# Kernel optimization log

Hardware: AMD Instinct MI355X
Metric: run time of the kernel (lower is better)

## Reference

```python
import jax, jax.numpy as jnp
import numpy as np

EPS = 1e-6


def _layernorm(x, g, b):
    mu = jnp.mean(x, axis=-1, keepdims=True)
    var = jnp.mean((x - mu) ** 2, axis=-1, keepdims=True)
    return (x - mu) * jax.lax.rsqrt(var + EPS) * g + b


def _sinusoidal_pe(seq_len, d_model):
    pos = jnp.arange(seq_len, dtype=jnp.float32)[:, None]
    div = jnp.exp(jnp.arange(0, d_model, 2, dtype=jnp.float32) * (-np.log(10000.0) / d_model))
    pe = jnp.zeros((seq_len, d_model), dtype=jnp.float32)
    pe = pe.at[:, 0::2].set(jnp.sin(pos * div))
    pe = pe.at[:, 1::2].set(jnp.cos(pos * div))
    return pe


def setup_inputs() -> dict:
    key = jax.random.key(0)
    ks = jax.random.split(key, 6)
    B, S, D, H = 4, 4096, 1024, 16
    std = 0.02
    return {
        "x": jax.random.normal(ks[0], (B, S, D), jnp.float32),
        "ln1_g": jnp.ones((D,), jnp.float32),
        "ln1_b": jnp.zeros((D,), jnp.float32),
        "w_qkv": jax.random.normal(ks[1], (D, 3 * D), jnp.float32) * std,
        "w_out": jax.random.normal(ks[2], (D, D), jnp.float32) * std,
        "b_out": jnp.zeros((D,), jnp.float32),
        "ln2_g": jnp.ones((D,), jnp.float32),
        "ln2_b": jnp.zeros((D,), jnp.float32),
        "w1": jax.random.normal(ks[3], (D, 2 * D), jnp.float32) * std,
        "b1": jnp.zeros((2 * D,), jnp.float32),
        "w2": jax.random.normal(ks[4], (2 * D, 2 * D), jnp.float32) * std,
        "b2": jnp.zeros((2 * D,), jnp.float32),
        "w3": jax.random.normal(ks[5], (2 * D, D), jnp.float32) * std,
        "b3": jnp.zeros((D,), jnp.float32),
    }


def reference(x, ln1_g, ln1_b, w_qkv, w_out, b_out, ln2_g, ln2_b, w1, b1, w2, b2, w3, b3):
    B, S, D = x.shape
    H = 16
    dh = D // H  # dim_head = 64

    h = _layernorm(x, ln1_g, ln1_b)
    h = h + _sinusoidal_pe(S, D)[None]  # space_dim == 1 -> sinusoidal PE

    # linear (kernelized, non-causal) self-attention: efficient-attention style
    qkv = h @ w_qkv  # [B,S,3D]
    q, k, v = jnp.split(qkv, 3, axis=-1)
    to_heads = lambda t: t.reshape(B, S, H, dh).transpose(0, 2, 1, 3)  # [B,H,S,dh]
    q, k, v = to_heads(q), to_heads(k), to_heads(v)
    q = jax.nn.softmax(q, axis=-1) * (dh ** -0.5)
    k = jax.nn.softmax(k, axis=2)  # softmax over sequence
    context = jnp.einsum('bhnd,bhne->bhde', k, v)  # [B,H,dh,dh]
    attn = jnp.einsum('bhnd,bhde->bhne', q, context)  # [B,H,S,dh]
    attn = attn.transpose(0, 2, 1, 3).reshape(B, S, D)
    attn = attn @ w_out + b_out

    x = x + attn  # residual (dropout p=0)

    y = _layernorm(x, ln2_g, ln2_b)
    y = jax.nn.gelu(y @ w1 + b1, approximate=False)
    y = jax.nn.gelu(y @ w2 + b2, approximate=False)
    y = y @ w3 + b3
    return x + y
```

## Files before the change

### kernel.cpp

```cpp
#include <hip/hip_runtime.h>
#include <cstdint>
#include <cstddef>

#define BB 4
#define SS 4096
#define DD 1024
#define HH 16
#define MM (BB*SS)

typedef __bf16 bf16x8 __attribute__((ext_vector_type(8)));
typedef float  f32x4  __attribute__((ext_vector_type(4)));

__device__ __forceinline__ float b2f(unsigned short h){
    union { unsigned int u; float f; } c; c.u = ((unsigned int)h) << 16; return c.f;
}
__device__ __forceinline__ float b2f_u(unsigned int u16){
    union { unsigned int u; float f; } c; c.u = u16 << 16; return c.f;
}
__device__ __forceinline__ unsigned short f2b(float f){
    union { float f; unsigned int u; } c; c.f = f;
    unsigned int u = c.u + 0x7FFFu + ((c.u >> 16) & 1u);
    return (unsigned short)(u >> 16);
}

__global__ __launch_bounds__(256) void transpose_cvt_all(
        const float* __restrict__ wqkv, const float* __restrict__ wout,
        const float* __restrict__ w1,   const float* __restrict__ w2,
        const float* __restrict__ w3,
        unsigned short* __restrict__ dqkv, unsigned short* __restrict__ dout,
        unsigned short* __restrict__ d1,   unsigned short* __restrict__ d2,
        unsigned short* __restrict__ d3)
{
    int id = blockIdx.x;
    const float* src; unsigned short* dst; int K, N, bx, by;
    if (id < 3072)       { src=wqkv; dst=dqkv; K=1024; N=3072; int r=id;        bx=r%96; by=r/96; }
    else if (id < 4096)  { src=wout; dst=dout; K=1024; N=1024; int r=id-3072;   bx=r%32; by=r/32; }
    else if (id < 6144)  { src=w1;   dst=d1;   K=1024; N=2048; int r=id-4096;   bx=r%64; by=r/64; }
    else if (id < 10240) { src=w2;   dst=d2;   K=2048; N=2048; int r=id-6144;   bx=r%64; by=r/64; }
    else                 { src=w3;   dst=d3;   K=2048; N=1024; int r=id-10240;  bx=r%32; by=r/32; }

    __shared__ float tile[32][33];
    int kb = by*32, nb = bx*32;
    int tx = threadIdx.x & 31, ty = threadIdx.x >> 5;
    for(int i=0;i<32;i+=8) tile[ty+i][tx] = src[(size_t)(kb+ty+i)*N + nb+tx];
    __syncthreads();
    for(int i=0;i<32;i+=8) dst[(size_t)(nb+ty+i)*K + kb+tx] = f2b(tile[tx][ty+i]);
}

template<int INBF>
__global__ __launch_bounds__(256) void ln_kernel(const void* __restrict__ xin,
                                                 const float* __restrict__ g,
                                                 const float* __restrict__ bta,
                                                 unsigned short* __restrict__ out,
                                                 int add_pe){
    int row = blockIdx.x;
    int t = threadIdx.x;
    float4 v;
    if (INBF == 0) {
        v = ((const float4*)((const float*)xin + (size_t)row*DD))[t];
    } else {
        ushort4 u = ((const ushort4*)((const unsigned short*)xin + (size_t)row*DD))[t];
        v.x = b2f(u.x); v.y = b2f(u.y); v.z = b2f(u.z); v.w = b2f(u.w);
    }
    float s = v.x+v.y+v.z+v.w;
    float q = v.x*v.x+v.y*v.y+v.z*v.z+v.w*v.w;
    for(int off=32; off>0; off>>=1){ s += __shfl_xor(s, off); q += __shfl_xor(q, off); }
    __shared__ float red[8];
    int wv = t>>6, ln = t&63;
    if(ln==0){ red[wv] = s; red[4+wv] = q; }
    __syncthreads();
    s = red[0]+red[1]+red[2]+red[3];
    q = red[4]+red[5]+red[6]+red[7];
    float mu = s * (1.0f/1024.0f);
    float var = q * (1.0f/1024.0f) - mu*mu;
    float rs = rsqrtf(var + 1e-6f);
    int d0 = t*4;
    float4 gg = ((const float4*)g)[t];
    float4 bb = ((const float4*)bta)[t];
    float o0 = (v.x-mu)*rs*gg.x + bb.x;
    float o1 = (v.y-mu)*rs*gg.y + bb.y;
    float o2 = (v.z-mu)*rs*gg.z + bb.z;
    float o3 = (v.w-mu)*rs*gg.w + bb.w;
    if(add_pe){
        int sidx = row & (SS-1);
        const float cfac = -0.008994473019508968f;
        float a0 = (float)sidx * expf(cfac * (float)(d0));
        float a1 = (float)sidx * expf(cfac * (float)(d0 + 2));
        o0 += sinf(a0); o1 += cosf(a0);
        o2 += sinf(a1); o3 += cosf(a1);
    }
    ushort4 o;
    o.x = f2b(o0); o.y = f2b(o1); o.z = f2b(o2); o.w = f2b(o3);
    *(ushort4*)(out + (size_t)row*DD + d0) = o;
}

template<int EPI>
__global__ __launch_bounds__(256, 4) void gemm_bt(
        const unsigned short* __restrict__ A,
        const unsigned short* __restrict__ Bt,
        void* __restrict__ Cout,
        const float* __restrict__ bias,
        const void* __restrict__ resid,
        int M, int N, int K)
{
    __shared__ __align__(16) unsigned short lA[128*64];
    __shared__ __align__(16) unsigned short lB[128*64];
    const int tid  = threadIdx.x;
    const int lane = tid & 63;
    const int wave = tid >> 6;
    const int quad = lane >> 4;
    const int l16  = lane & 15;
    const int wr = wave >> 1, wc = wave & 1;

    int gn  = gridDim.x;
    int lin = blockIdx.y * gn + blockIdx.x;
    int xcd = lin & 7;
    int j   = lin >> 3;
    int mt  = xcd + 8*(j/gn);
    int nt  = j - (j/gn)*gn;
    const int m0 = mt * 128;
    const int n0 = nt * 128;

    f32x4 acc[4][4] = {};

    for (int k0 = 0; k0 < K; k0 += 64) {
        __syncthreads();
        #pragma unroll
        for (int i = 0; i < 4; i++) {
            int c   = tid + 256*i;
            int row = c >> 3;
            int kc  = ((c & 7) ^ (row & 7)) << 3;
            const unsigned short* gA = A  + (size_t)(m0 + row) * K + k0 + kc;
            const unsigned short* gB = Bt + (size_t)(n0 + row) * K + k0 + kc;
            char* lpA = ((char*)lA) + (wave<<10) + (i<<12);
            char* lpB = ((char*)lB) + (wave<<10) + (i<<12);
            __builtin_amdgcn_global_load_lds((const __attribute__((address_space(1))) void*)gA,
                                             (__attribute__((address_space(3))) void*)lpA, 16, 0, 0);
            __builtin_amdgcn_global_load_lds((const __attribute__((address_space(1))) void*)gB,
                                             (__attribute__((address_space(3))) void*)lpB, 16, 0, 0);
        }
        __syncthreads();
        #pragma unroll
        for (int kk = 0; kk < 2; kk++) {
            bf16x8 af[4], bfr[4];
            #pragma unroll
            for (int mi = 0; mi < 4; mi++) {
                int row = wr*64 + mi*16 + l16;
                int kb  = (kk*64 + quad*16) ^ ((row & 7) << 4);
                af[mi] = *(const bf16x8*)((const char*)lA + row*128 + kb);
            }
            #pragma unroll
            for (int ni = 0; ni < 4; ni++) {
                int row = wc*64 + ni*16 + l16;
                int kb  = (kk*64 + quad*16) ^ ((row & 7) << 4);
                bfr[ni] = *(const bf16x8*)((const char*)lB + row*128 + kb);
            }
            #pragma unroll
            for (int mi = 0; mi < 4; mi++)
                #pragma unroll
                for (int ni = 0; ni < 4; ni++)
                    acc[mi][ni] = __builtin_amdgcn_mfma_f32_16x16x32_bf16(af[mi], bfr[ni], acc[mi][ni], 0, 0, 0);
        }
    }

    #pragma unroll
    for (int mi = 0; mi < 4; mi++) {
        #pragma unroll
        for (int r = 0; r < 4; r++) {
            int grow = m0 + wr*64 + mi*16 + quad*4 + r;
            #pragma unroll
            for (int ni = 0; ni < 4; ni++) {
                int gcol = n0 + wc*64 + ni*16 + l16;
                float v = acc[mi][ni][r];
                size_t idx = (size_t)grow * N + gcol;
                if (EPI == 0) {
                    ((unsigned short*)Cout)[idx] = f2b(v);
                } else if (EPI == 1) {
                    v += bias[gcol];
                    v = 0.5f * v * (1.0f + erff(v * 0.70710678118654752f));
                    ((unsigned short*)Cout)[idx] = f2b(v);
                } else if (EPI == 2) {
                    v += bias[gcol] + ((const float*)resid)[idx];
                    ((unsigned short*)Cout)[idx] = f2b(v);
                } else {
                    v += bias[gcol] + b2f(((const unsigned short*)resid)[idx]);
                    ((float*)Cout)[idx] = v;
                }
            }
        }
    }
}

__global__ __launch_bounds__(256) void ctx_partial(const unsigned short* __restrict__ qkv,
                                                   float* __restrict__ EP,
                                                   float* __restrict__ CS){
    int sc = blockIdx.x, h = blockIdx.y, b = blockIdx.z;
    int t = threadIdx.x;
    __shared__ __align__(16) float kl[64][64];
    __shared__ __align__(16) float vl[64][64];
    __shared__ float csred[4][64];
    float acc[4][4] = {};
    float cspart = 0.0f;
    int e4 = (t & 15) * 4, d4 = (t >> 4) * 4;
    int dcol = t & 63, schunk = t >> 6;
    for(int s0 = 0; s0 < 256; s0 += 64){
        __syncthreads();
        #pragma unroll
        for(int j=0;j<2;j++){
            int lin = t + 256*j;
            int row = lin >> 3;
            int c8  = (lin & 7) * 8;
            size_t gr = (size_t)(b*SS + sc*256 + s0 + row);
            uint4 kv = *(const uint4*)(qkv + gr*3072 + DD + h*64 + c8);
            float4 ka, kb2;
            ka.x = expf(b2f_u(kv.x & 0xFFFFu)); ka.y = expf(b2f_u(kv.x >> 16));
            ka.z = expf(b2f_u(kv.y & 0xFFFFu)); ka.w = expf(b2f_u(kv.y >> 16));
            kb2.x = expf(b2f_u(kv.z & 0xFFFFu)); kb2.y = expf(b2f_u(kv.z >> 16));
            kb2.z = expf(b2f_u(kv.w & 0xFFFFu)); kb2.w = expf(b2f_u(kv.w >> 16));
            *(float4*)&kl[row][c8]   = ka;
            *(float4*)&kl[row][c8+4] = kb2;
            uint4 vv = *(const uint4*)(qkv + gr*3072 + 2*DD + h*64 + c8);
            float4 va, vb;
            va.x = b2f_u(vv.x & 0xFFFFu); va.y = b2f_u(vv.x >> 16);
            va.z = b2f_u(vv.y & 0xFFFFu); va.w = b2f_u(vv.y >> 16);
            vb.x = b2f_u(vv.z & 0xFFFFu); vb.y = b2f_u(vv.z >> 16);
            vb.z = b2f_u(vv.w & 0xFFFFu); vb.w = b2f_u(vv.w >> 16);
            *(float4*)&vl[row][c8]   = va;
            *(float4*)&vl[row][c8+4] = vb;
        }
        __syncthreads();
        #pragma unroll
        for(int i=0;i<16;i++) cspart += kl[schunk*16+i][dcol];
        for(int s=0;s<64;s++){
            float4 k4 = *(const float4*)&kl[s][d4];
            float4 v4 = *(const float4*)&vl[s][e4];
            acc[0][0] += k4.x*v4.x; acc[0][1] += k4.x*v4.y; acc[0][2] += k4.x*v4.z; acc[0][3] += k4.x*v4.w;
            acc[1][0] += k4.y*v4.x; acc[1][1] += k4.y*v4.y; acc[1][2] += k4.y*v4.z; acc[1][3] += k4.y*v4.w;
            acc[2][0] += k4.z*v4.x; acc[2][1] += k4.z*v4.y; acc[2][2] += k4.z*v4.z; acc[2][3] += k4.z*v4.w;
            acc[3][0] += k4.w*v4.x; acc[3][1] += k4.w*v4.y; acc[3][2] += k4.w*v4.z; acc[3][3] += k4.w*v4.w;
        }
    }
    int slot = (b*HH + h)*16 + sc;
    float* ep = EP + (size_t)slot*4096;
    #pragma unroll
    for(int i=0;i<4;i++)
        *(float4*)&ep[(d4+i)*64 + e4] = *(float4*)&acc[i][0];
    csred[schunk][dcol] = cspart;
    __syncthreads();
    if(t < 64) CS[slot*64 + t] = csred[0][t]+csred[1][t]+csred[2][t]+csred[3][t];
}

__global__ __launch_bounds__(256) void ctx_reduce(const float* __restrict__ EP,
                                                  const float* __restrict__ CS,
                                                  float* __restrict__ CTXF){
    int bh = blockIdx.x;
    int t = threadIdx.x;
    int d = t >> 2, e0 = (t & 3) * 16;
    float cs = 0.0f;
    #pragma unroll
    for(int sl=0; sl<16; sl++) cs += CS[(bh*16+sl)*64 + d];
    float inv = 1.0f/cs;
    #pragma unroll
    for(int i=0;i<16;i++){
        float s = 0.0f;
        #pragma unroll
        for(int sl=0; sl<16; sl++) s += EP[(size_t)(bh*16+sl)*4096 + d*64 + e0 + i];
        CTXF[(size_t)bh*4096 + d*64 + e0 + i] = s * inv;
    }
}

__global__ __launch_bounds__(256) void attn_heads(const unsigned short* __restrict__ qkv,
                                                  const float* __restrict__ CTXF,
                                                  unsigned short* __restrict__ abuf){
    int rg = blockIdx.x, h = blockIdx.y;
    int b = rg >> 6;
    int t = threadIdx.x;
    __shared__ __align__(16) float cl[64][64];
    __shared__ __align__(16) float qlT[64*68];
    const float* cb = CTXF + (size_t)(b*HH + h)*4096;
    for(int j=0;j<4;j++){
        int lin = t + 256*j;
        ((float4*)cl)[lin] = ((const float4*)cb)[lin];
    }
    {
        int r = t >> 2, seg = (t & 3) * 16;
        const unsigned short* qp = qkv + (size_t)(rg*64 + r)*3072 + h*64 + seg;
        float vals[16];
        float m = -1e30f;
        #pragma unroll
        for(int u=0; u<4; u++){
            ushort4 qv = *(const ushort4*)(qp + u*4);
            vals[u*4+0]=b2f(qv.x); vals[u*4+1]=b2f(qv.y); vals[u*4+2]=b2f(qv.z); vals[u*4+3]=b2f(qv.w);
        }
        #pragma unroll
        for(int i=0;i<16;i++) m = fmaxf(m, vals[i]);
        m = fmaxf(m, __shfl_xor(m, 1));
        m = fmaxf(m, __shfl_xor(m, 2));
        float ssum = 0.0f;
        #pragma unroll
        for(int i=0;i<16;i++){ vals[i] = expf(vals[i]-m); ssum += vals[i]; }
        ssum += __shfl_xor(ssum, 1);
        ssum += __shfl_xor(ssum, 2);
        float scl = 0.125f/ssum;
        #pragma unroll
        for(int i=0;i<16;i++) qlT[(seg+i)*68 + r] = vals[i]*scl;
    }
    __syncthreads();
    int e4 = (t & 15) * 4, r4 = (t >> 4) * 4;
    float acc[4][4] = {};
    for(int d=0; d<64; d++){
        float4 q4 = *(const float4*)&qlT[d*68 + r4];
        float4 c4 = *(const float4*)&cl[d][e4];
        acc[0][0] += q4.x*c4.x; acc[0][1] += q4.x*c4.y; acc[0][2] += q4.x*c4.z; acc[0][3] += q4.x*c4.w;
        acc[1][0] += q4.y*c4.x; acc[1][1] += q4.y*c4.y; acc[1][2] += q4.y*c4.z; acc[1][3] += q4.y*c4.w;
        acc[2][0] += q4.z*c4.x; acc[2][1] += q4.z*c4.y; acc[2][2] += q4.z*c4.z; acc[2][3] += q4.z*c4.w;
        acc[3][0] += q4.w*c4.x; acc[3][1] += q4.w*c4.y; acc[3][2] += q4.w*c4.z; acc[3][3] += q4.w*c4.w;
    }
    #pragma unroll
    for(int i=0;i<4;i++){
        ushort4 o;
        o.x = f2b(acc[i][0]); o.y = f2b(acc[i][1]); o.z = f2b(acc[i][2]); o.w = f2b(acc[i][3]);
        *(ushort4*)(abuf + (size_t)(rg*64 + r4 + i)*DD + h*64 + e4) = o;
    }
}

extern "C" void kernel_launch(void* const* d_in, const int* in_sizes, int n_in,
                              void* d_out, int out_size, void* d_ws, size_t ws_size,
                              hipStream_t stream)
{
    const float* x     = (const float*)d_in[0];
    const float* ln1_g = (const float*)d_in[1];
    const float* ln1_b = (const float*)d_in[2];
    const float* w_qkv = (const float*)d_in[3];
    const float* w_out = (const float*)d_in[4];
    const float* b_out = (const float*)d_in[5];
    const float* ln2_g = (const float*)d_in[6];
    const float* ln2_b = (const float*)d_in[7];
    const float* w1    = (const float*)d_in[8];
    const float* b1    = (const float*)d_in[9];
    const float* w2    = (const float*)d_in[10];
    const float* b2    = (const float*)d_in[11];
    const float* w3    = (const float*)d_in[12];
    const float* b3    = (const float*)d_in[13];

    char* ws = (char*)d_ws;
    unsigned short* wqkvT = (unsigned short*)(ws + 0);
    unsigned short* woutT = (unsigned short*)(ws + 6291456);
    unsigned short* w1T   = (unsigned short*)(ws + 8388608);
    unsigned short* w2T   = (unsigned short*)(ws + 12582912);
    unsigned short* w3T   = (unsigned short*)(ws + 20971520);
    unsigned short* Hbuf  = (unsigned short*)(ws + 25165824);
    unsigned short* QKV   = (unsigned short*)(ws + 58720256);
    float*          EP    = (float*)(ws + 159383552);
    float*          CS    = (float*)(ws + 176160768);
    float*          CTXF  = (float*)(ws + 176422912);
    unsigned short* Abuf  = Hbuf;
    unsigned short* X2    = (unsigned short*)(ws + 58720256);
    unsigned short* H2    = Hbuf;
    unsigned short* Y1    = (unsigned short*)d_out;
    unsigned short* Y2    = (unsigned short*)(ws + 125829120);

    transpose_cvt_all<<<12288, 256, 0, stream>>>(w_qkv, w_out, w1, w2, w3,
                                                 wqkvT, woutT, w1T, w2T, w3T);

    ln_kernel<0><<<MM, 256, 0, stream>>>(x, ln1_g, ln1_b, Hbuf, 1);

    gemm_bt<0><<<dim3(3072/128, MM/128), 256, 0, stream>>>(Hbuf, wqkvT, QKV, nullptr, nullptr, MM, 3072, 1024);

    ctx_partial<<<dim3(16, HH, BB), 256, 0, stream>>>(QKV, EP, CS);
    ctx_reduce<<<BB*HH, 256, 0, stream>>>(EP, CS, CTXF);
    attn_heads<<<dim3(256, HH), 256, 0, stream>>>(QKV, CTXF, Abuf);

    gemm_bt<2><<<dim3(1024/128, MM/128), 256, 0, stream>>>(Abuf, woutT, X2, b_out, x, MM, 1024, 1024);

    ln_kernel<1><<<MM, 256, 0, stream>>>(X2, ln2_g, ln2_b, H2, 0);

    gemm_bt<1><<<dim3(2048/128, MM/128), 256, 0, stream>>>(H2, w1T, Y1, b1, nullptr, MM, 2048, 1024);
    gemm_bt<1><<<dim3(2048/128, MM/128), 256, 0, stream>>>(Y1, w2T, Y2, b2, nullptr, MM, 2048, 2048);
    gemm_bt<3><<<dim3(1024/128, MM/128), 256, 0, stream>>>(Y2, w3T, d_out, b3, X2, MM, 1024, 2048);
}
```

Baseline: 741.0 us.

## Use single-wave blocks with 8x8 register tiles for attention kernels

Rewrites ctx_partial and attn_heads to run one 64-thread wave per block, each lane computing an 8x8 outer-product tile and doing a full per-row softmax without shuffles or a cross-wave reduction. It also relaxes the GEMM launch bound from 4 to 2 blocks per SM, giving the compiler more registers. The aim is more reuse per LDS load and fewer syncs, at the cost of fewer threads in flight for the small kernels. Unpadded qT[d][l] writes may cause LDS bank conflicts, and the 64-element vals array raises register pressure.

```diff
diff --git a/kernel.cpp b/kernel.cpp
--- a/kernel.cpp
+++ b/kernel.cpp
@@ -95,7 +95,7 @@
 }
 
 template<int EPI>
-__global__ __launch_bounds__(256, 4) void gemm_bt(
+__global__ __launch_bounds__(256, 2) void gemm_bt(
         const unsigned short* __restrict__ A,
         const unsigned short* __restrict__ Bt,
         void* __restrict__ Cout,
@@ -191,23 +191,21 @@
     }
 }
 
-__global__ __launch_bounds__(256) void ctx_partial(const unsigned short* __restrict__ qkv,
-                                                   float* __restrict__ EP,
-                                                   float* __restrict__ CS){
+__global__ __launch_bounds__(64) void ctx_partial(const unsigned short* __restrict__ qkv,
+                                                  float* __restrict__ EP,
+                                                  float* __restrict__ CS){
     int sc = blockIdx.x, h = blockIdx.y, b = blockIdx.z;
-    int t = threadIdx.x;
+    int l = threadIdx.x;
     __shared__ __align__(16) float kl[64][64];
     __shared__ __align__(16) float vl[64][64];
-    __shared__ float csred[4][64];
-    float acc[4][4] = {};
-    float cspart = 0.0f;
-    int e4 = (t & 15) * 4, d4 = (t >> 4) * 4;
-    int dcol = t & 63, schunk = t >> 6;
+    float acc[8][8] = {};
+    float csacc = 0.0f;
+    const int d8 = (l >> 3) * 8, e8 = (l & 7) * 8;
     for(int s0 = 0; s0 < 256; s0 += 64){
         __syncthreads();
         #pragma unroll
-        for(int j=0;j<2;j++){
-            int lin = t + 256*j;
+        for(int j=0;j<8;j++){
+            int lin = l + 64*j;
             int row = lin >> 3;
             int c8  = (lin & 7) * 8;
             size_t gr = (size_t)(b*SS + sc*256 + s0 + row);
@@ -229,25 +227,33 @@
             *(float4*)&vl[row][c8+4] = vb;
         }
         __syncthreads();
-        #pragma unroll
-        for(int i=0;i<16;i++) cspart += kl[schunk*16+i][dcol];
+        #pragma unroll 8
+        for(int s=0;s<64;s++) csacc += kl[s][l];
         for(int s=0;s<64;s++){
-            float4 k4 = *(const float4*)&kl[s][d4];
-            float4 v4 = *(const float4*)&vl[s][e4];
-            acc[0][0] += k4.x*v4.x; acc[0][1] += k4.x*v4.y; acc[0][2] += k4.x*v4.z; acc[0][3] += k4.x*v4.w;
-            acc[1][0] += k4.y*v4.x; acc[1][1] += k4.y*v4.y; acc[1][2] += k4.y*v4.z; acc[1][3] += k4.y*v4.w;
-            acc[2][0] += k4.z*v4.x; acc[2][1] += k4.z*v4.y; acc[2][2] += k4.z*v4.z; acc[2][3] += k4.z*v4.w;
-            acc[3][0] += k4.w*v4.x; acc[3][1] += k4.w*v4.y; acc[3][2] += k4.w*v4.z; acc[3][3] += k4.w*v4.w;
+            float4 ka = *(const float4*)&kl[s][d8];
+            float4 kb2 = *(const float4*)&kl[s][d8+4];
+            float4 va = *(const float4*)&vl[s][e8];
+            float4 vb = *(const float4*)&vl[s][e8+4];
+            float kv8[8] = {ka.x,ka.y,ka.z,ka.w,kb2.x,kb2.y,kb2.z,kb2.w};
+            float vv8[8] = {va.x,va.y,va.z,va.w,vb.x,vb.y,vb.z,vb.w};
+            #pragma unroll
+            for(int i=0;i<8;i++)
+                #pragma unroll
+                for(int jj=0;jj<8;jj++)
+                    acc[i][jj] += kv8[i]*vv8[jj];
         }
     }
     int slot = (b*HH + h)*16 + sc;
     float* ep = EP + (size_t)slot*4096;
     #pragma unroll
-    for(int i=0;i<4;i++)
-        *(float4*)&ep[(d4+i)*64 + e4] = *(float4*)&acc[i][0];
-    csred[schunk][dcol] = cspart;
-    __syncthreads();
-    if(t < 64) CS[slot*64 + t] = csred[0][t]+csred[1][t]+csred[2][t]+csred[3][t];
+    for(int i=0;i<8;i++){
+        float4 o1, o2;
+        o1.x=acc[i][0]; o1.y=acc[i][1]; o1.z=acc[i][2]; o1.w=acc[i][3];
+        o2.x=acc[i][4]; o2.y=acc[i][5]; o2.z=acc[i][6]; o2.w=acc[i][7];
+        *(float4*)&ep[(d8+i)*64 + e8]     = o1;
+        *(float4*)&ep[(d8+i)*64 + e8 + 4] = o2;
+    }
+    CS[slot*64 + l] = csacc;
 }
 
 __global__ __launch_bounds__(256) void ctx_reduce(const float* __restrict__ EP,
@@ -269,58 +275,62 @@
     }
 }
 
-__global__ __launch_bounds__(256) void attn_heads(const unsigned short* __restrict__ qkv,
-                                                  const float* __restrict__ CTXF,
-                                                  unsigned short* __restrict__ abuf){
+__global__ __launch_bounds__(64) void attn_heads(const unsigned short* __restrict__ qkv,
+                                                 const float* __restrict__ CTXF,
+                                                 unsigned short* __restrict__ abuf){
     int rg = blockIdx.x, h = blockIdx.y;
     int b = rg >> 6;
-    int t = threadIdx.x;
+    int l = threadIdx.x;
     __shared__ __align__(16) float cl[64][64];
-    __shared__ __align__(16) float qlT[64*68];
+    __shared__ __align__(16) float qT[64][64];
     const float* cb = CTXF + (size_t)(b*HH + h)*4096;
-    for(int j=0;j<4;j++){
-        int lin = t + 256*j;
+    #pragma unroll
+    for(int j=0;j<16;j++){
+        int lin = l + 64*j;
         ((float4*)cl)[lin] = ((const float4*)cb)[lin];
     }
     {
-        int r = t >> 2, seg = (t & 3) * 16;
-        const unsigned short* qp = qkv + (size_t)(rg*64 + r)*3072 + h*64 + seg;
-        float vals[16];
-        float m = -1e30f;
-        #pragma unroll
-        for(int u=0; u<4; u++){
+        const unsigned short* qp = qkv + (size_t)(rg*64 + l)*3072 + h*64;
+        float vals[64];
+        #pragma unroll
+        for(int u=0; u<16; u++){
             ushort4 qv = *(const ushort4*)(qp + u*4);
             vals[u*4+0]=b2f(qv.x); vals[u*4+1]=b2f(qv.y); vals[u*4+2]=b2f(qv.z); vals[u*4+3]=b2f(qv.w);
         }
-        #pragma unroll
-        for(int i=0;i<16;i++) m = fmaxf(m, vals[i]);
-        m = fmaxf(m, __shfl_xor(m, 1));
-        m = fmaxf(m, __shfl_xor(m, 2));
+        float m = vals[0];
+        #pragma unroll
+        for(int i=1;i<64;i++) m = fmaxf(m, vals[i]);
         float ssum = 0.0f;
         #pragma unroll
-        for(int i=0;i<16;i++){ vals[i] = expf(vals[i]-m); ssum += vals[i]; }
-        ssum += __shfl_xor(ssum, 1);
-        ssum += __shfl_xor(ssum, 2);
+        for(int i=0;i<64;i++){ vals[i] = expf(vals[i]-m); ssum += vals[i]; }
         float scl = 0.125f/ssum;
         #pragma unroll
-        for(int i=0;i<16;i++) qlT[(seg+i)*68 + r] = vals[i]*scl;
+        for(int d=0; d<64; d++) qT[d][l] = vals[d]*scl;
     }
     __syncthreads();
-    int e4 = (t & 15) * 4, r4 = (t >> 4) * 4;
-    float acc[4][4] = {};
+    const int r8 = (l >> 3) * 8, e8 = (l & 7) * 8;
+    float acc[8][8] = {};
     for(int d=0; d<64; d++){
-        float4 q4 = *(const float4*)&qlT[d*68 + r4];
-        float4 c4 = *(const float4*)&cl[d][e4];
-        acc[0][0] += q4.x*c4.x; acc[0][1] += q4.x*c4.y; acc[0][2] += q4.x*c4.z; acc[0][3] += q4.x*c4.w;
-        acc[1][0] += q4.y*c4.x; acc[1][1] += q4.y*c4.y; acc[1][2] += q4.y*c4.z; acc[1][3] += q4.y*c4.w;
-        acc[2][0] += q4.z*c4.x; acc[2][1] += q4.z*c4.y; acc[2][2] += q4.z*c4.z; acc[2][3] += q4.z*c4.w;
-        acc[3][0] += q4.w*c4.x; acc[3][1] += q4.w*c4.y; acc[3][2] += q4.w*c4.z; acc[3][3] += q4.w*c4.w;
-    }
-    #pragma unroll
-    for(int i=0;i<4;i++){
-        ushort4 o;
-        o.x = f2b(acc[i][0]); o.y = f2b(acc[i][1]); o.z = f2b(acc[i][2]); o.w = f2b(acc[i][3]);
-        *(ushort4*)(abuf + (size_t)(rg*64 + r4 + i)*DD + h*64 + e4) = o;
+        float4 qa = *(const float4*)&qT[d][r8];
+        float4 qb = *(const float4*)&qT[d][r8+4];
+        float4 ca = *(const float4*)&cl[d][e8];
+        float4 cb2 = *(const float4*)&cl[d][e8+4];
+        float q8[8] = {qa.x,qa.y,qa.z,qa.w,qb.x,qb.y,qb.z,qb.w};
+        float c8v[8] = {ca.x,ca.y,ca.z,ca.w,cb2.x,cb2.y,cb2.z,cb2.w};
+        #pragma unroll
+        for(int i=0;i<8;i++)
+            #pragma unroll
+            for(int jj=0;jj<8;jj++)
+                acc[i][jj] += q8[i]*c8v[jj];
+    }
+    #pragma unroll
+    for(int i=0;i<8;i++){
+        ushort4 o1, o2;
+        o1.x = f2b(acc[i][0]); o1.y = f2b(acc[i][1]); o1.z = f2b(acc[i][2]); o1.w = f2b(acc[i][3]);
+        o2.x = f2b(acc[i][4]); o2.y = f2b(acc[i][5]); o2.z = f2b(acc[i][6]); o2.w = f2b(acc[i][7]);
+        unsigned short* op = abuf + (size_t)(rg*64 + r8 + i)*DD + h*64 + e8;
+        *(ushort4*)op       = o1;
+        *(ushort4*)(op + 4) = o2;
     }
 }
 
@@ -367,9 +377,9 @@
 
     gemm_bt<0><<<dim3(3072/128, MM/128), 256, 0, stream>>>(Hbuf, wqkvT, QKV, nullptr, nullptr, MM, 3072, 1024);
 
-    ctx_partial<<<dim3(16, HH, BB), 256, 0, stream>>>(QKV, EP, CS);
+    ctx_partial<<<dim3(16, HH, BB), 64, 0, stream>>>(QKV, EP, CS);
     ctx_reduce<<<BB*HH, 256, 0, stream>>>(EP, CS, CTXF);
-    attn_heads<<<dim3(256, HH), 256, 0, stream>>>(QKV, CTXF, Abuf);
+    attn_heads<<<dim3(256, HH), 64, 0, stream>>>(QKV, CTXF, Abuf);
 
     gemm_bt<2><<<dim3(1024/128, MM/128), 256, 0, stream>>>(Abuf, woutT, X2, b_out, x, MM, 1024, 1024);
 
```

Measured after the change: 748.8 us. About the same (+1.1%).
